# Performance work log

Hardware: AMD Instinct MI355X
Metric: run time of the kernel (lower is better)

Reference implementation:

```python
import jax, jax.numpy as jnp
import numpy as np

NEG_SLOPE = 0.2


def gat_conv(x, src, dst, W, a_src, a_dst, b, heads, out_ch, concat):
    """PyG-style GATConv (eval mode, self-loops already appended to src/dst)."""
    N = x.shape[0]
    h = (x @ W).reshape(N, heads, out_ch)            # [N,H,C]
    alpha_s = jnp.einsum('nhc,hc->nh', h, a_src)     # [N,H]
    alpha_d = jnp.einsum('nhc,hc->nh', h, a_dst)
    e = jax.nn.leaky_relu(alpha_s[src] + alpha_d[dst], NEG_SLOPE)  # [E,H]
    # segment softmax over incoming edges per destination node
    m = jax.ops.segment_max(e, dst, num_segments=N)  # every node has a self loop
    ex = jnp.exp(e - m[dst])
    denom = jax.ops.segment_sum(ex, dst, num_segments=N)
    alpha = ex / (denom[dst] + 1e-16)                # [E,H]
    msg = h[src] * alpha[:, :, None]                 # [E,H,C]
    out = jax.ops.segment_sum(msg, dst, num_segments=N)  # [N,H,C]
    if concat:
        out = out.reshape(N, heads * out_ch)
    else:
        out = out.mean(axis=1)
    return out + b


def setup_inputs() -> dict:
    key = jax.random.key(0)
    ks = jax.random.split(key, 12)
    N, E, F_IN = 100000, 3200000, 512
    H1, C1 = 8, 8           # conv1: heads=8, out=8, concat -> 64
    H2, C2 = 8, 16          # conv2: heads=8, out=num_classes=16, mean over heads
    x = jax.random.normal(ks[0], (N, F_IN), dtype=jnp.float32)
    edge_index = jax.random.randint(ks[1], (2, E), 0, N, dtype=jnp.int32)
    g = lambda k, s, fan: jax.random.normal(k, s, dtype=jnp.float32) / np.sqrt(fan)
    return {
        'x': x,
        'edge_index': edge_index,
        'W1': g(ks[2], (F_IN, H1 * C1), F_IN),
        'a_src1': g(ks[3], (H1, C1), C1),
        'a_dst1': g(ks[4], (H1, C1), C1),
        'b1': jnp.zeros((H1 * C1,), jnp.float32),
        'W2': g(ks[5], (H1 * C1, H2 * C2), H1 * C1),
        'a_src2': g(ks[6], (H2, C2), C2),
        'a_dst2': g(ks[7], (H2, C2), C2),
        'b2': jnp.zeros((C2,), jnp.float32),
    }


def reference(x, edge_index, W1, a_src1, a_dst1, b1, W2, a_src2, a_dst2, b2):
    N = x.shape[0]
    loops = jnp.arange(N, dtype=edge_index.dtype)
    src = jnp.concatenate([edge_index[0], loops])
    dst = jnp.concatenate([edge_index[1], loops])
    h = gat_conv(x, src, dst, W1, a_src1, a_dst1, b1, heads=8, out_ch=8, concat=True)
    h = jax.nn.elu(h)
    out = gat_conv(h, src, dst, W2, a_src2, a_dst2, b2, heads=8, out_ch=16, concat=False)
    return out
```

## Files before the change

### kernel.cpp

```cpp
#include <hip/hip_runtime.h>
#include <hip/hip_bf16.h>
#include <hip/hip_fp16.h>
#include <cstddef>

#define NEG_SLOPE 0.2f

typedef _Float16 half8 __attribute__((ext_vector_type(8)));
typedef float floatx4 __attribute__((ext_vector_type(4)));
typedef float floatx2 __attribute__((ext_vector_type(2)));


__global__ __launch_bounds__(256) void bucket_hist_k(const int* __restrict__ dst, int E,
                                                     int* __restrict__ bhist, int NB) {
    __shared__ int lh[256];
    for (int t = threadIdx.x; t < 256; t += 256) lh[t] = 0;
    __syncthreads();
    int per = (E + gridDim.x - 1) / gridDim.x;
    int s = blockIdx.x * per;
    int e = min(s + per, E);
    for (int i = s + threadIdx.x; i < e; i += 256) atomicAdd(&lh[dst[i] >> 9], 1);
    __syncthreads();
    for (int t = threadIdx.x; t < NB; t += 256)
        if (lh[t]) atomicAdd(&bhist[t], lh[t]);
}

__global__ __launch_bounds__(256) void bucket_scan_k(const int* __restrict__ bhist, int NB,
                                                     int* __restrict__ bbase, int* __restrict__ cursor,
                                                     int* __restrict__ row_start, int N, int E) {
    __shared__ int tmp[256];
    int tid = threadIdx.x;
    int v = (tid < NB) ? bhist[tid] : 0;
    tmp[tid] = v;
    __syncthreads();
    for (int d = 1; d < 256; d <<= 1) {
        int t = tmp[tid];
        int a = (tid >= d) ? tmp[tid - d] : 0;
        __syncthreads();
        tmp[tid] = t + a;
        __syncthreads();
    }
    if (tid < NB) {
        int b = tmp[tid] - v;
        bbase[tid] = b;
        cursor[tid] = b;
    }
    if (tid == 0) {
        bbase[NB] = E;
        row_start[N] = E;
    }
}

__global__ __launch_bounds__(256) void partition_k(const int* __restrict__ src,
                                                   const int* __restrict__ dst, int E,
                                                   int* __restrict__ cursor,
                                                   unsigned int* __restrict__ part, int NB) {
    __shared__ int lh[256];
    __shared__ int lbase[256];
    for (int t = threadIdx.x; t < 256; t += 256) lh[t] = 0;
    __syncthreads();
    int per = (E + gridDim.x - 1) / gridDim.x;
    int s = blockIdx.x * per;
    int e = min(s + per, E);
    for (int i = s + threadIdx.x; i < e; i += 256) atomicAdd(&lh[dst[i] >> 9], 1);
    __syncthreads();
    for (int t = threadIdx.x; t < NB; t += 256) {
        int c = lh[t];
        lbase[t] = c ? atomicAdd(&cursor[t], c) : 0;
        lh[t] = 0;
    }
    __syncthreads();
    for (int i = s + threadIdx.x; i < e; i += 256) {
        int d = dst[i];
        int b = d >> 9;
        int lo = atomicAdd(&lh[b], 1);
        part[lbase[b] + lo] = ((unsigned)src[i] << 9) | (unsigned)(d & 511);
    }
}

__global__ __launch_bounds__(512) void bucket_build_k(const unsigned int* __restrict__ part,
                                                      const int* __restrict__ bbase,
                                                      int* __restrict__ row_start,
                                                      int* __restrict__ csr, int N) {
    __shared__ int cnt[512];
    __shared__ int cur[512];
    int b = blockIdx.x, tid = threadIdx.x;
    int n0 = b << 9;
    int s = bbase[b], e2 = bbase[b + 1];
    cnt[tid] = 0;
    __syncthreads();
    for (int i = s + tid; i < e2; i += 512) atomicAdd(&cnt[part[i] & 511], 1);
    __syncthreads();
    int v = cnt[tid];
    for (int d = 1; d < 512; d <<= 1) {
        int t = cnt[tid];
        int a = (tid >= d) ? cnt[tid - d] : 0;
        __syncthreads();
        cnt[tid] = t + a;
        __syncthreads();
    }
    int excl = cnt[tid] - v;
    if (n0 + tid < N) row_start[n0 + tid] = s + excl;
    cur[tid] = excl;
    __syncthreads();
    for (int i = s + tid; i < e2; i += 512) {
        unsigned u = part[i];
        int p = atomicAdd(&cur[u & 511], 1);
        csr[s + p] = (int)(u >> 9);
    }
}


__global__ void convw_k(const float* __restrict__ W, _Float16* __restrict__ WT,
                        int K, int Nc) {
    int i = blockIdx.x * 256 + threadIdx.x;
    if (i < K * Nc) {
        int k = i / Nc, n = i % Nc;
        WT[(size_t)n * K + k] = (_Float16)W[i];
    }
}


__global__ __launch_bounds__(256) void gemm1_k(const float* __restrict__ A,
                                               const _Float16* __restrict__ BT,
                                               const float* __restrict__ a_s,
                                               const float* __restrict__ a_d,
                                               __half* __restrict__ C,
                                               float* __restrict__ os,
                                               float* __restrict__ od, int M) {
    constexpr int NT = 4, K = 512, Nc = 64;
    int wave = threadIdx.x >> 6, lane = threadIdx.x & 63;
    int m16 = lane & 15, quad = lane >> 4;
    int arow = blockIdx.x * 64 + wave * 16 + m16;
    int arc = arow < M ? arow : M - 1;
    floatx4 acc[NT] = {};
    for (int k0 = 0; k0 < K; k0 += 32) {
        const float* ap = A + (size_t)arc * K + k0 + quad * 8;
        float4 v0 = *(const float4*)ap;
        float4 v1 = *(const float4*)(ap + 4);
        half8 af;
        af[0] = (_Float16)v0.x; af[1] = (_Float16)v0.y;
        af[2] = (_Float16)v0.z; af[3] = (_Float16)v0.w;
        af[4] = (_Float16)v1.x; af[5] = (_Float16)v1.y;
        af[6] = (_Float16)v1.z; af[7] = (_Float16)v1.w;
#pragma unroll
        for (int t = 0; t < NT; ++t) {
            half8 bf = *(const half8*)(BT + (size_t)(t * 16 + m16) * K + k0 + quad * 8);
            acc[t] = __builtin_amdgcn_mfma_f32_16x16x32_f16(af, bf, acc[t], 0, 0, 0);
        }
    }
    int gm0 = blockIdx.x * 64 + wave * 16 + quad * 4;
    int head = (m16 >> 3);
#pragma unroll
    for (int t = 0; t < NT; ++t) {
        float ws = a_s[(2 * t + head) * 8 + (m16 & 7)];
        float wd = a_d[(2 * t + head) * 8 + (m16 & 7)];
#pragma unroll
        for (int r = 0; r < 4; ++r) {
            int gm = gm0 + r;
            float v = acc[t][r];
            if (gm < M) C[(size_t)gm * Nc + t * 16 + m16] = __float2half(v);
            float s = v * ws, d = v * wd;
            s += __shfl_xor(s, 1, 64); d += __shfl_xor(d, 1, 64);
            s += __shfl_xor(s, 2, 64); d += __shfl_xor(d, 2, 64);
            s += __shfl_xor(s, 4, 64); d += __shfl_xor(d, 4, 64);
            if ((m16 & 7) == 0 && gm < M) {
                os[gm * 8 + 2 * t + head] = s;
                od[gm * 8 + 2 * t + head] = d;
            }
        }
    }
}


__global__ __launch_bounds__(256) void gemm2_k(const _Float16* __restrict__ A,
                                               const _Float16* __restrict__ BT,
                                               const float* __restrict__ a_s,
                                               const float* __restrict__ a_d,
                                               unsigned short* __restrict__ Cf8,
                                               float* __restrict__ os,
                                               float* __restrict__ od, int M) {
    constexpr int NT = 8, K = 64;
    int wave = threadIdx.x >> 6, lane = threadIdx.x & 63;
    int m16 = lane & 15, quad = lane >> 4;
    int arow = blockIdx.x * 64 + wave * 16 + m16;
    int arc = arow < M ? arow : M - 1;
    floatx4 acc[NT] = {};
    for (int k0 = 0; k0 < K; k0 += 32) {
        half8 af = *(const half8*)(A + (size_t)arc * K + k0 + quad * 8);
#pragma unroll
        for (int t = 0; t < NT; ++t) {
            half8 bf = *(const half8*)(BT + (size_t)(t * 16 + m16) * K + k0 + quad * 8);
            acc[t] = __builtin_amdgcn_mfma_f32_16x16x32_f16(af, bf, acc[t], 0, 0, 0);
        }
    }
    int gm0 = blockIdx.x * 64 + wave * 16 + quad * 4;
#pragma unroll
    for (int t = 0; t < NT; ++t) {
        float ws = a_s[t * 16 + m16];
        float wd = a_d[t * 16 + m16];
#pragma unroll
        for (int r = 0; r < 4; ++r) {
            int gm = gm0 + r;
            float v = acc[t][r];
            float o = __shfl_xor(v, 1, 64);
            if (gm < M && !(m16 & 1)) {
                unsigned p = __builtin_amdgcn_cvt_pk_fp8_f32(v, o, 0, false);
                Cf8[(size_t)gm * 64 + t * 8 + (m16 >> 1)] = (unsigned short)(p & 0xffff);
            }
            float s = v * ws, d = v * wd;
            s += __shfl_xor(s, 1, 64); d += __shfl_xor(d, 1, 64);
            s += __shfl_xor(s, 2, 64); d += __shfl_xor(d, 2, 64);
            s += __shfl_xor(s, 4, 64); d += __shfl_xor(d, 4, 64);
            s += __shfl_xor(s, 8, 64); d += __shfl_xor(d, 8, 64);
            if (gm < M && m16 == t) {
                os[gm * 8 + t] = s;
                od[gm * 8 + t] = d;
            }
        }
    }
}


__global__ __launch_bounds__(64) void aggregate1_k(
    const __half2* __restrict__ H1, const float* __restrict__ as,
    const float* __restrict__ ad, const int* __restrict__ row_start,
    const int* __restrict__ csr, const float* __restrict__ b1,
    __half2* __restrict__ h1o, int N) {
    int l = threadIdx.x;
    int ll = l & 31;
    int n = min(blockIdx.x * 2 + (l >> 5), N - 1);
    int h = ll >> 2;
    int jj = ll & 3;
    int hbase = (l & 32) | (ll & 28);
    float adv = ad[n * 8 + h];
    float e0 = as[n * 8 + h] + adv;
    e0 = fmaxf(e0, NEG_SLOPE * e0);
    float ex0 = __expf(e0);
    float denom = ex0;
    float2 self = __half22float2(H1[(size_t)n * 32 + ll]);
    float accx = ex0 * self.x, accy = ex0 * self.y;
    int e = row_start[n], end = row_start[n + 1];
    for (; e + 8 <= end; e += 8) {
        int sjA = csr[e + jj];
        int sjB = csr[e + 4 + jj];
        float tA = as[sjA * 8 + h] + adv; tA = fmaxf(tA, NEG_SLOPE * tA);
        float tB = as[sjB * 8 + h] + adv; tB = fmaxf(tB, NEG_SLOPE * tB);
        float xA = __expf(tA), xB = __expf(tB);
#pragma unroll
        for (int q = 0; q < 4; ++q) {
            int sqA = __shfl(sjA, hbase + q, 64);
            float xqA = __shfl(xA, hbase + q, 64);
            float2 vA = __half22float2(H1[(size_t)sqA * 32 + ll]);
            int sqB = __shfl(sjB, hbase + q, 64);
            float xqB = __shfl(xB, hbase + q, 64);
            float2 vB = __half22float2(H1[(size_t)sqB * 32 + ll]);
            denom += xqA + xqB;
            accx = fmaf(xqA, vA.x, accx); accy = fmaf(xqA, vA.y, accy);
            accx = fmaf(xqB, vB.x, accx); accy = fmaf(xqB, vB.y, accy);
        }
    }
    while (e < end) {
        int rem = min(end - e, 4);
        int sj = csr[e + min(jj, rem - 1)];
        float t = as[sj * 8 + h] + adv;
        t = fmaxf(t, NEG_SLOPE * t);
        float xj = __expf(t);
        for (int q = 0; q < rem; ++q) {
            int sq = __shfl(sj, hbase + q, 64);
            float xq = __shfl(xj, hbase + q, 64);
            float2 v = __half22float2(H1[(size_t)sq * 32 + ll]);
            denom += xq;
            accx = fmaf(xq, v.x, accx);
            accy = fmaf(xq, v.y, accy);
        }
        e += rem;
    }
    float vx = accx / denom + b1[2 * ll];
    float vy = accy / denom + b1[2 * ll + 1];
    vx = vx > 0.f ? vx : expm1f(vx);
    vy = vy > 0.f ? vy : expm1f(vy);
    h1o[(size_t)n * 32 + ll] = __floats2half2_rn(vx, vy);
}


__global__ __launch_bounds__(64) void aggregate2_k(
    const unsigned int* __restrict__ H2, const float* __restrict__ as,
    const float* __restrict__ ad, const int* __restrict__ row_start,
    const int* __restrict__ csr, const float* __restrict__ b2,
    float* __restrict__ out, int N) {
    int l = threadIdx.x;
    int ll = l & 31;
    int n = min(blockIdx.x * 2 + (l >> 5), N - 1);
    int h = ll >> 2;
    int jj = ll & 3;
    int hbase = (l & 32) | (ll & 28);
    float adv = ad[n * 8 + h];
    float e0 = as[n * 8 + h] + adv;
    e0 = fmaxf(e0, NEG_SLOPE * e0);
    float ex0 = __expf(e0);
    float denom = ex0;
    unsigned sv = H2[(size_t)n * 32 + ll];
    floatx2 s01 = __builtin_amdgcn_cvt_pk_f32_fp8((int)sv, false);
    floatx2 s23 = __builtin_amdgcn_cvt_pk_f32_fp8((int)sv, true);
    float a0 = ex0 * s01[0], a1 = ex0 * s01[1];
    float a2 = ex0 * s23[0], a3 = ex0 * s23[1];
    int e = row_start[n], end = row_start[n + 1];
    for (; e + 8 <= end; e += 8) {
        int sjA = csr[e + jj];
        int sjB = csr[e + 4 + jj];
        float tA = as[sjA * 8 + h] + adv; tA = fmaxf(tA, NEG_SLOPE * tA);
        float tB = as[sjB * 8 + h] + adv; tB = fmaxf(tB, NEG_SLOPE * tB);
        float xA = __expf(tA), xB = __expf(tB);
#pragma unroll
        for (int q = 0; q < 4; ++q) {
            int sqA = __shfl(sjA, hbase + q, 64);
            float xqA = __shfl(xA, hbase + q, 64);
            unsigned gvA = H2[(size_t)sqA * 32 + ll];
            int sqB = __shfl(sjB, hbase + q, 64);
            float xqB = __shfl(xB, hbase + q, 64);
            unsigned gvB = H2[(size_t)sqB * 32 + ll];
            floatx2 vA01 = __builtin_amdgcn_cvt_pk_f32_fp8((int)gvA, false);
            floatx2 vA23 = __builtin_amdgcn_cvt_pk_f32_fp8((int)gvA, true);
            floatx2 vB01 = __builtin_amdgcn_cvt_pk_f32_fp8((int)gvB, false);
            floatx2 vB23 = __builtin_amdgcn_cvt_pk_f32_fp8((int)gvB, true);
            denom += xqA + xqB;
            a0 = fmaf(xqA, vA01[0], a0); a1 = fmaf(xqA, vA01[1], a1);
            a2 = fmaf(xqA, vA23[0], a2); a3 = fmaf(xqA, vA23[1], a3);
            a0 = fmaf(xqB, vB01[0], a0); a1 = fmaf(xqB, vB01[1], a1);
            a2 = fmaf(xqB, vB23[0], a2); a3 = fmaf(xqB, vB23[1], a3);
        }
    }
    while (e < end) {
        int rem = min(end - e, 4);
        int sj = csr[e + min(jj, rem - 1)];
        float t = as[sj * 8 + h] + adv;
        t = fmaxf(t, NEG_SLOPE * t);
        float xj = __expf(t);
        for (int q = 0; q < rem; ++q) {
            int sq = __shfl(sj, hbase + q, 64);
            float xq = __shfl(xj, hbase + q, 64);
            unsigned gv = H2[(size_t)sq * 32 + ll];
            floatx2 v01 = __builtin_amdgcn_cvt_pk_f32_fp8((int)gv, false);
            floatx2 v23 = __builtin_amdgcn_cvt_pk_f32_fp8((int)gv, true);
            denom += xq;
            a0 = fmaf(xq, v01[0], a0); a1 = fmaf(xq, v01[1], a1);
            a2 = fmaf(xq, v23[0], a2); a3 = fmaf(xq, v23[1], a3);
        }
        e += rem;
    }
    float inv = 1.f / denom;
    a0 *= inv; a1 *= inv; a2 *= inv; a3 *= inv;
#pragma unroll
    for (int m = 4; m <= 16; m <<= 1) {
        a0 += __shfl_xor(a0, m, 64);
        a1 += __shfl_xor(a1, m, 64);
        a2 += __shfl_xor(a2, m, 64);
        a3 += __shfl_xor(a3, m, 64);
    }
    if (ll < 4) {
        int c0 = ll * 4;
        float4 o;
        o.x = a0 * 0.125f + b2[c0];
        o.y = a1 * 0.125f + b2[c0 + 1];
        o.z = a2 * 0.125f + b2[c0 + 2];
        o.w = a3 * 0.125f + b2[c0 + 3];
        *(float4*)(out + (size_t)n * 16 + c0) = o;
    }
}


extern "C" void kernel_launch(void* const* d_in, const int* in_sizes, int n_in,
                              void* d_out, int out_size, void* d_ws, size_t ws_size,
                              hipStream_t stream) {
    (void)n_in; (void)out_size; (void)ws_size;
    const float* x      = (const float*)d_in[0];
    const int*   ei     = (const int*)d_in[1];
    const float* W1     = (const float*)d_in[2];
    const float* a_src1 = (const float*)d_in[3];
    const float* a_dst1 = (const float*)d_in[4];
    const float* b1     = (const float*)d_in[5];
    const float* W2     = (const float*)d_in[6];
    const float* a_src2 = (const float*)d_in[7];
    const float* a_dst2 = (const float*)d_in[8];
    const float* b2     = (const float*)d_in[9];

    int N = in_sizes[0] / 512;
    int E = in_sizes[1] / 2;
    const int* src = ei;
    const int* dst = ei + E;
    int NB = (N + 511) >> 9;

    char* ws = (char*)d_ws;
    size_t off = 0;
    auto alloc = [&](size_t bytes) -> void* {
        void* p = ws + off;
        off = (off + bytes + 255) & ~(size_t)255;
        return p;
    };
    __half* h1  = (__half*)alloc((size_t)N * 64 * 2);
    __half* h1o = (__half*)alloc((size_t)N * 64 * 2);
    unsigned short* h2f8 = (unsigned short*)alloc((size_t)N * 64 * 2);
    float* as1  = (float*)alloc((size_t)N * 8 * 4);
    float* ad1  = (float*)alloc((size_t)N * 8 * 4);
    float* as2  = (float*)alloc((size_t)N * 8 * 4);
    float* ad2  = (float*)alloc((size_t)N * 8 * 4);
    _Float16* W1T = (_Float16*)alloc((size_t)512 * 64 * 2);
    _Float16* W2T = (_Float16*)alloc((size_t)64 * 128 * 2);
    int* row_start = (int*)alloc((size_t)(N + 1) * 4);
    int* bhist     = (int*)alloc(256 * 4);
    int* bbase     = (int*)alloc(257 * 4);
    int* cursor    = (int*)alloc(256 * 4);
    unsigned int* part = (unsigned int*)alloc((size_t)E * 4);
    int* csr       = (int*)alloc((size_t)E * 4);

    convw_k<<<(512 * 64 + 255) / 256, 256, 0, stream>>>(W1, W1T, 512, 64);
    convw_k<<<(64 * 128 + 255) / 256, 256, 0, stream>>>(W2, W2T, 64, 128);

    hipMemsetAsync(bhist, 0, 256 * 4, stream);
    bucket_hist_k<<<512, 256, 0, stream>>>(dst, E, bhist, NB);
    bucket_scan_k<<<1, 256, 0, stream>>>(bhist, NB, bbase, cursor, row_start, N, E);
    partition_k<<<512, 256, 0, stream>>>(src, dst, E, cursor, part, NB);
    bucket_build_k<<<NB, 512, 0, stream>>>(part, bbase, row_start, csr, N);

    int gblocks = (N + 63) / 64;
    int ablocks = (N + 1) / 2;

    gemm1_k<<<gblocks, 256, 0, stream>>>(x, W1T, a_src1, a_dst1, h1, as1, ad1, N);
    aggregate1_k<<<ablocks, 64, 0, stream>>>((const __half2*)h1, as1, ad1, row_start,
                                             csr, b1, (__half2*)h1o, N);

    gemm2_k<<<gblocks, 256, 0, stream>>>((const _Float16*)h1o, W2T, a_src2, a_dst2,
                                         h2f8, as2, ad2, N);
    aggregate2_k<<<ablocks, 64, 0, stream>>>((const unsigned int*)h2f8, as2, ad2,
                                             row_start, csr, b2, (float*)d_out, N);
}
```

Before: 651.7 us.

## Fuse preprocessing kernels, co-launch partition with gemm1, and rework aggregation lane mapping

```diff
diff --git a/kernel.cpp b/kernel.cpp
--- a/kernel.cpp
+++ b/kernel.cpp
@@ -10,18 +10,35 @@
 typedef float floatx2 __attribute__((ext_vector_type(2)));
 
 
-__global__ __launch_bounds__(256) void bucket_hist_k(const int* __restrict__ dst, int E,
-                                                     int* __restrict__ bhist, int NB) {
-    __shared__ int lh[256];
-    for (int t = threadIdx.x; t < 256; t += 256) lh[t] = 0;
-    __syncthreads();
-    int per = (E + gridDim.x - 1) / gridDim.x;
-    int s = blockIdx.x * per;
-    int e = min(s + per, E);
-    for (int i = s + threadIdx.x; i < e; i += 256) atomicAdd(&lh[dst[i] >> 9], 1);
-    __syncthreads();
-    for (int t = threadIdx.x; t < NB; t += 256)
-        if (lh[t]) atomicAdd(&bhist[t], lh[t]);
+__global__ __launch_bounds__(256) void pre_k(const int* __restrict__ dst, int E,
+                                             int* __restrict__ bhist, int NB,
+                                             const float* __restrict__ W1, _Float16* __restrict__ W1T,
+                                             const float* __restrict__ W2, _Float16* __restrict__ W2T) {
+    int b = blockIdx.x;
+    if (b < 512) {
+        __shared__ int lh[256];
+        for (int t = threadIdx.x; t < 256; t += 256) lh[t] = 0;
+        __syncthreads();
+        int per = (E + 511) / 512;
+        int s = b * per;
+        int e = min(s + per, E);
+        for (int i = s + threadIdx.x; i < e; i += 256) atomicAdd(&lh[dst[i] >> 9], 1);
+        __syncthreads();
+        for (int t = threadIdx.x; t < NB; t += 256)
+            if (lh[t]) atomicAdd(&bhist[t], lh[t]);
+    } else if (b < 640) {
+        int i = (b - 512) * 256 + threadIdx.x;
+        if (i < 512 * 64) {
+            int k = i / 64, n = i % 64;
+            W1T[(size_t)n * 512 + k] = (_Float16)W1[i];
+        }
+    } else {
+        int i = (b - 640) * 256 + threadIdx.x;
+        if (i < 64 * 128) {
+            int k = i / 128, n = i % 128;
+            W2T[(size_t)n * 64 + k] = (_Float16)W2[i];
+        }
+    }
 }
 
 __global__ __launch_bounds__(256) void bucket_scan_k(const int* __restrict__ bhist, int NB,
@@ -47,33 +64,6 @@
     if (tid == 0) {
         bbase[NB] = E;
         row_start[N] = E;
-    }
-}
-
-__global__ __launch_bounds__(256) void partition_k(const int* __restrict__ src,
-                                                   const int* __restrict__ dst, int E,
-                                                   int* __restrict__ cursor,
-                                                   unsigned int* __restrict__ part, int NB) {
-    __shared__ int lh[256];
-    __shared__ int lbase[256];
-    for (int t = threadIdx.x; t < 256; t += 256) lh[t] = 0;
-    __syncthreads();
-    int per = (E + gridDim.x - 1) / gridDim.x;
-    int s = blockIdx.x * per;
-    int e = min(s + per, E);
-    for (int i = s + threadIdx.x; i < e; i += 256) atomicAdd(&lh[dst[i] >> 9], 1);
-    __syncthreads();
-    for (int t = threadIdx.x; t < NB; t += 256) {
-        int c = lh[t];
-        lbase[t] = c ? atomicAdd(&cursor[t], c) : 0;
-        lh[t] = 0;
-    }
-    __syncthreads();
-    for (int i = s + threadIdx.x; i < e; i += 256) {
-        int d = dst[i];
-        int b = d >> 9;
-        int lo = atomicAdd(&lh[b], 1);
-        part[lbase[b] + lo] = ((unsigned)src[i] << 9) | (unsigned)(d & 511);
     }
 }
 
@@ -110,27 +100,41 @@
 }
 
 
-__global__ void convw_k(const float* __restrict__ W, _Float16* __restrict__ WT,
-                        int K, int Nc) {
-    int i = blockIdx.x * 256 + threadIdx.x;
-    if (i < K * Nc) {
-        int k = i / Nc, n = i % Nc;
-        WT[(size_t)n * K + k] = (_Float16)W[i];
-    }
-}
-
-
-__global__ __launch_bounds__(256) void gemm1_k(const float* __restrict__ A,
-                                               const _Float16* __restrict__ BT,
-                                               const float* __restrict__ a_s,
-                                               const float* __restrict__ a_d,
-                                               __half* __restrict__ C,
-                                               float* __restrict__ os,
-                                               float* __restrict__ od, int M) {
+__global__ __launch_bounds__(256) void gemm1_part_k(
+    const float* __restrict__ A, const _Float16* __restrict__ BT,
+    const float* __restrict__ a_s, const float* __restrict__ a_d,
+    __half* __restrict__ C, float* __restrict__ os, float* __restrict__ od, int M,
+    const int* __restrict__ src, const int* __restrict__ dst, int E,
+    int* __restrict__ cursor, unsigned int* __restrict__ part, int NB) {
+    if (blockIdx.x < 512) {
+        __shared__ int lh[256];
+        __shared__ int lbase[256];
+        for (int t = threadIdx.x; t < 256; t += 256) lh[t] = 0;
+        __syncthreads();
+        int per = (E + 511) / 512;
+        int s = blockIdx.x * per;
+        int e = min(s + per, E);
+        for (int i = s + threadIdx.x; i < e; i += 256) atomicAdd(&lh[dst[i] >> 9], 1);
+        __syncthreads();
+        for (int t = threadIdx.x; t < NB; t += 256) {
+            int c = lh[t];
+            lbase[t] = c ? atomicAdd(&cursor[t], c) : 0;
+            lh[t] = 0;
+        }
+        __syncthreads();
+        for (int i = s + threadIdx.x; i < e; i += 256) {
+            int d = dst[i];
+            int b = d >> 9;
+            int lo = atomicAdd(&lh[b], 1);
+            part[lbase[b] + lo] = ((unsigned)src[i] << 9) | (unsigned)(d & 511);
+        }
+        return;
+    }
     constexpr int NT = 4, K = 512, Nc = 64;
+    int bid = blockIdx.x - 512;
     int wave = threadIdx.x >> 6, lane = threadIdx.x & 63;
     int m16 = lane & 15, quad = lane >> 4;
-    int arow = blockIdx.x * 64 + wave * 16 + m16;
+    int arow = bid * 64 + wave * 16 + m16;
     int arc = arow < M ? arow : M - 1;
     floatx4 acc[NT] = {};
     for (int k0 = 0; k0 < K; k0 += 32) {
@@ -148,7 +152,7 @@
             acc[t] = __builtin_amdgcn_mfma_f32_16x16x32_f16(af, bf, acc[t], 0, 0, 0);
         }
     }
-    int gm0 = blockIdx.x * 64 + wave * 16 + quad * 4;
+    int gm0 = bid * 64 + wave * 16 + quad * 4;
     int head = (m16 >> 3);
 #pragma unroll
     for (int t = 0; t < NT; ++t) {
@@ -221,150 +225,184 @@
 }
 
 
-__global__ __launch_bounds__(64) void aggregate1_k(
-    const __half2* __restrict__ H1, const float* __restrict__ as,
+__global__ __launch_bounds__(256) void aggregate1_k(
+    const uint2* __restrict__ H1, const float* __restrict__ as,
     const float* __restrict__ ad, const int* __restrict__ row_start,
     const int* __restrict__ csr, const float* __restrict__ b1,
-    __half2* __restrict__ h1o, int N) {
-    int l = threadIdx.x;
+    uint2* __restrict__ h1o, int N) {
+    int l = threadIdx.x & 63;
+    int wv = threadIdx.x >> 6;
     int ll = l & 31;
-    int n = min(blockIdx.x * 2 + (l >> 5), N - 1);
-    int h = ll >> 2;
-    int jj = ll & 3;
-    int hbase = (l & 32) | (ll & 28);
+    int n = min((int)(blockIdx.x * 8 + wv * 2 + (l >> 5)), N - 1);
+    int k = ll & 15;
+    int jj = ll >> 4;
+    int h = k >> 1;
+
     float adv = ad[n * 8 + h];
     float e0 = as[n * 8 + h] + adv;
     e0 = fmaxf(e0, NEG_SLOPE * e0);
     float ex0 = __expf(e0);
-    float denom = ex0;
-    float2 self = __half22float2(H1[(size_t)n * 32 + ll]);
-    float accx = ex0 * self.x, accy = ex0 * self.y;
+    float x0 = jj ? 0.f : ex0;
+
+    uint2 sv = H1[(size_t)n * 16 + k];
+    float2 s01 = __half22float2(*(const __half2*)&sv.x);
+    float2 s23 = __half22float2(*(const __half2*)&sv.y);
+    float denom = x0;
+    float a0 = x0 * s01.x, a1 = x0 * s01.y, a2 = x0 * s23.x, a3 = x0 * s23.y;
+
     int e = row_start[n], end = row_start[n + 1];
     for (; e + 8 <= end; e += 8) {
-        int sjA = csr[e + jj];
-        int sjB = csr[e + 4 + jj];
-        float tA = as[sjA * 8 + h] + adv; tA = fmaxf(tA, NEG_SLOPE * tA);
-        float tB = as[sjB * 8 + h] + adv; tB = fmaxf(tB, NEG_SLOPE * tB);
-        float xA = __expf(tA), xB = __expf(tB);
-#pragma unroll
-        for (int q = 0; q < 4; ++q) {
-            int sqA = __shfl(sjA, hbase + q, 64);
-            float xqA = __shfl(xA, hbase + q, 64);
-            float2 vA = __half22float2(H1[(size_t)sqA * 32 + ll]);
-            int sqB = __shfl(sjB, hbase + q, 64);
-            float xqB = __shfl(xB, hbase + q, 64);
-            float2 vB = __half22float2(H1[(size_t)sqB * 32 + ll]);
-            denom += xqA + xqB;
-            accx = fmaf(xqA, vA.x, accx); accy = fmaf(xqA, vA.y, accy);
-            accx = fmaf(xqB, vB.x, accx); accy = fmaf(xqB, vB.y, accy);
-        }
-    }
-    while (e < end) {
-        int rem = min(end - e, 4);
-        int sj = csr[e + min(jj, rem - 1)];
-        float t = as[sj * 8 + h] + adv;
-        t = fmaxf(t, NEG_SLOPE * t);
-        float xj = __expf(t);
-        for (int q = 0; q < rem; ++q) {
-            int sq = __shfl(sj, hbase + q, 64);
-            float xq = __shfl(xj, hbase + q, 64);
-            float2 v = __half22float2(H1[(size_t)sq * 32 + ll]);
-            denom += xq;
-            accx = fmaf(xq, v.x, accx);
-            accy = fmaf(xq, v.y, accy);
-        }
-        e += rem;
-    }
-    float vx = accx / denom + b1[2 * ll];
-    float vy = accy / denom + b1[2 * ll + 1];
-    vx = vx > 0.f ? vx : expm1f(vx);
-    vy = vy > 0.f ? vy : expm1f(vy);
-    h1o[(size_t)n * 32 + ll] = __floats2half2_rn(vx, vy);
-}
-
-
-__global__ __launch_bounds__(64) void aggregate2_k(
-    const unsigned int* __restrict__ H2, const float* __restrict__ as,
+#pragma unroll
+        for (int u = 0; u < 4; ++u) {
+            int sj = csr[e + 2 * u + jj];
+            float t = as[sj * 8 + h] + adv;
+            t = fmaxf(t, NEG_SLOPE * t);
+            float x = __expf(t);
+            uint2 gv = H1[(size_t)sj * 16 + k];
+            float2 v01 = __half22float2(*(const __half2*)&gv.x);
+            float2 v23 = __half22float2(*(const __half2*)&gv.y);
+            denom += x;
+            a0 = fmaf(x, v01.x, a0); a1 = fmaf(x, v01.y, a1);
+            a2 = fmaf(x, v23.x, a2); a3 = fmaf(x, v23.y, a3);
+        }
+    }
+    if (e < end) {
+#pragma unroll
+        for (int u = 0; u < 4; ++u) {
+            int idx = e + 2 * u + jj;
+            int sj = csr[min(idx, end - 1)];
+            float t = as[sj * 8 + h] + adv;
+            t = fmaxf(t, NEG_SLOPE * t);
+            float x = idx < end ? __expf(t) : 0.f;
+            uint2 gv = H1[(size_t)sj * 16 + k];
+            float2 v01 = __half22float2(*(const __half2*)&gv.x);
+            float2 v23 = __half22float2(*(const __half2*)&gv.y);
+            denom += x;
+            a0 = fmaf(x, v01.x, a0); a1 = fmaf(x, v01.y, a1);
+            a2 = fmaf(x, v23.x, a2); a3 = fmaf(x, v23.y, a3);
+        }
+    }
+    denom += __shfl_xor(denom, 16, 64);
+    a0 += __shfl_xor(a0, 16, 64);
+    a1 += __shfl_xor(a1, 16, 64);
+    a2 += __shfl_xor(a2, 16, 64);
+    a3 += __shfl_xor(a3, 16, 64);
+    float inv = 1.f / denom;
+    float r0 = a0 * inv + b1[4 * k + 0];
+    float r1 = a1 * inv + b1[4 * k + 1];
+    float r2 = a2 * inv + b1[4 * k + 2];
+    float r3 = a3 * inv + b1[4 * k + 3];
+    r0 = r0 > 0.f ? r0 : expm1f(r0);
+    r1 = r1 > 0.f ? r1 : expm1f(r1);
+    r2 = r2 > 0.f ? r2 : expm1f(r2);
+    r3 = r3 > 0.f ? r3 : expm1f(r3);
+    if (!jj) {
+        __half2 p01 = __floats2half2_rn(r0, r1);
+        __half2 p23 = __floats2half2_rn(r2, r3);
+        uint2 o;
+        o.x = *(const unsigned*)&p01;
+        o.y = *(const unsigned*)&p23;
+        h1o[(size_t)n * 16 + k] = o;
+    }
+}
+
+
+__global__ __launch_bounds__(256) void aggregate2_k(
+    const uint2* __restrict__ H2, const float* __restrict__ as,
     const float* __restrict__ ad, const int* __restrict__ row_start,
     const int* __restrict__ csr, const float* __restrict__ b2,
     float* __restrict__ out, int N) {
-    int l = threadIdx.x;
+    int l = threadIdx.x & 63;
+    int wv = threadIdx.x >> 6;
     int ll = l & 31;
-    int n = min(blockIdx.x * 2 + (l >> 5), N - 1);
-    int h = ll >> 2;
-    int jj = ll & 3;
-    int hbase = (l & 32) | (ll & 28);
+    int n = min((int)(blockIdx.x * 8 + wv * 2 + (l >> 5)), N - 1);
+    int k = ll & 15;
+    int jj = ll >> 4;
+    int h = k >> 1;
+
     float adv = ad[n * 8 + h];
     float e0 = as[n * 8 + h] + adv;
     e0 = fmaxf(e0, NEG_SLOPE * e0);
     float ex0 = __expf(e0);
-    float denom = ex0;
-    unsigned sv = H2[(size_t)n * 32 + ll];
-    floatx2 s01 = __builtin_amdgcn_cvt_pk_f32_fp8((int)sv, false);
-    floatx2 s23 = __builtin_amdgcn_cvt_pk_f32_fp8((int)sv, true);
-    float a0 = ex0 * s01[0], a1 = ex0 * s01[1];
-    float a2 = ex0 * s23[0], a3 = ex0 * s23[1];
+    float x0 = jj ? 0.f : ex0;
+
+    uint2 sv = H2[(size_t)n * 16 + k];
+    floatx2 p01 = __builtin_amdgcn_cvt_pk_f32_fp8((int)sv.x, false);
+    floatx2 p23 = __builtin_amdgcn_cvt_pk_f32_fp8((int)sv.x, true);
+    floatx2 p45 = __builtin_amdgcn_cvt_pk_f32_fp8((int)sv.y, false);
+    floatx2 p67 = __builtin_amdgcn_cvt_pk_f32_fp8((int)sv.y, true);
+    float denom = x0;
+    float a0 = x0 * p01[0], a1 = x0 * p01[1], a2 = x0 * p23[0], a3 = x0 * p23[1];
+    float a4 = x0 * p45[0], a5 = x0 * p45[1], a6 = x0 * p67[0], a7 = x0 * p67[1];
+
     int e = row_start[n], end = row_start[n + 1];
     for (; e + 8 <= end; e += 8) {
-        int sjA = csr[e + jj];
-        int sjB = csr[e + 4 + jj];
-        float tA = as[sjA * 8 + h] + adv; tA = fmaxf(tA, NEG_SLOPE * tA);
-        float tB = as[sjB * 8 + h] + adv; tB = fmaxf(tB, NEG_SLOPE * tB);
-        float xA = __expf(tA), xB = __expf(tB);
-#pragma unroll
-        for (int q = 0; q < 4; ++q) {
-            int sqA = __shfl(sjA, hbase + q, 64);
-            float xqA = __shfl(xA, hbase + q, 64);
-            unsigned gvA = H2[(size_t)sqA * 32 + ll];
-            int sqB = __shfl(sjB, hbase + q, 64);
-            float xqB = __shfl(xB, hbase + q, 64);
-            unsigned gvB = H2[(size_t)sqB * 32 + ll];
-            floatx2 vA01 = __builtin_amdgcn_cvt_pk_f32_fp8((int)gvA, false);
-            floatx2 vA23 = __builtin_amdgcn_cvt_pk_f32_fp8((int)gvA, true);
-            floatx2 vB01 = __builtin_amdgcn_cvt_pk_f32_fp8((int)gvB, false);
-            floatx2 vB23 = __builtin_amdgcn_cvt_pk_f32_fp8((int)gvB, true);
-            denom += xqA + xqB;
-            a0 = fmaf(xqA, vA01[0], a0); a1 = fmaf(xqA, vA01[1], a1);
-            a2 = fmaf(xqA, vA23[0], a2); a3 = fmaf(xqA, vA23[1], a3);
-            a0 = fmaf(xqB, vB01[0], a0); a1 = fmaf(xqB, vB01[1], a1);
-            a2 = fmaf(xqB, vB23[0], a2); a3 = fmaf(xqB, vB23[1], a3);
-        }
-    }
-    while (e < end) {
-        int rem = min(end - e, 4);
-        int sj = csr[e + min(jj, rem - 1)];
-        float t = as[sj * 8 + h] + adv;
-        t = fmaxf(t, NEG_SLOPE * t);
-        float xj = __expf(t);
-        for (int q = 0; q < rem; ++q) {
-            int sq = __shfl(sj, hbase + q, 64);
-            float xq = __shfl(xj, hbase + q, 64);
-            unsigned gv = H2[(size_t)sq * 32 + ll];
-            floatx2 v01 = __builtin_amdgcn_cvt_pk_f32_fp8((int)gv, false);
-            floatx2 v23 = __builtin_amdgcn_cvt_pk_f32_fp8((int)gv, true);
-            denom += xq;
-            a0 = fmaf(xq, v01[0], a0); a1 = fmaf(xq, v01[1], a1);
-            a2 = fmaf(xq, v23[0], a2); a3 = fmaf(xq, v23[1], a3);
-        }
-        e += rem;
-    }
+#pragma unroll
+        for (int u = 0; u < 4; ++u) {
+            int sj = csr[e + 2 * u + jj];
+            float t = as[sj * 8 + h] + adv;
+            t = fmaxf(t, NEG_SLOPE * t);
+            float x = __expf(t);
+            uint2 gv = H2[(size_t)sj * 16 + k];
+            floatx2 v01 = __builtin_amdgcn_cvt_pk_f32_fp8((int)gv.x, false);
+            floatx2 v23 = __builtin_amdgcn_cvt_pk_f32_fp8((int)gv.x, true);
+            floatx2 v45 = __builtin_amdgcn_cvt_pk_f32_fp8((int)gv.y, false);
+            floatx2 v67 = __builtin_amdgcn_cvt_pk_f32_fp8((int)gv.y, true);
+            denom += x;
+            a0 = fmaf(x, v01[0], a0); a1 = fmaf(x, v01[1], a1);
+            a2 = fmaf(x, v23[0], a2); a3 = fmaf(x, v23[1], a3);
+            a4 = fmaf(x, v45[0], a4); a5 = fmaf(x, v45[1], a5);
+            a6 = fmaf(x, v67[0], a6); a7 = fmaf(x, v67[1], a7);
+        }
+    }
+    if (e < end) {
+#pragma unroll
+        for (int u = 0; u < 4; ++u) {
+            int idx = e + 2 * u + jj;
+            int sj = csr[min(idx, end - 1)];
+            float t = as[sj * 8 + h] + adv;
+            t = fmaxf(t, NEG_SLOPE * t);
+            float x = idx < end ? __expf(t) : 0.f;
+            uint2 gv = H2[(size_t)sj * 16 + k];
+            floatx2 v01 = __builtin_amdgcn_cvt_pk_f32_fp8((int)gv.x, false);
+            floatx2 v23 = __builtin_amdgcn_cvt_pk_f32_fp8((int)gv.x, true);
+            floatx2 v45 = __builtin_amdgcn_cvt_pk_f32_fp8((int)gv.y, false);
+            floatx2 v67 = __builtin_amdgcn_cvt_pk_f32_fp8((int)gv.y, true);
+            denom += x;
+            a0 = fmaf(x, v01[0], a0); a1 = fmaf(x, v01[1], a1);
+            a2 = fmaf(x, v23[0], a2); a3 = fmaf(x, v23[1], a3);
+            a4 = fmaf(x, v45[0], a4); a5 = fmaf(x, v45[1], a5);
+            a6 = fmaf(x, v67[0], a6); a7 = fmaf(x, v67[1], a7);
+        }
+    }
+    denom += __shfl_xor(denom, 16, 64);
     float inv = 1.f / denom;
     a0 *= inv; a1 *= inv; a2 *= inv; a3 *= inv;
-#pragma unroll
-    for (int m = 4; m <= 16; m <<= 1) {
+    a4 *= inv; a5 *= inv; a6 *= inv; a7 *= inv;
+#pragma unroll
+    for (int m = 2; m <= 16; m <<= 1) {
         a0 += __shfl_xor(a0, m, 64);
         a1 += __shfl_xor(a1, m, 64);
         a2 += __shfl_xor(a2, m, 64);
         a3 += __shfl_xor(a3, m, 64);
-    }
-    if (ll < 4) {
-        int c0 = ll * 4;
-        float4 o;
-        o.x = a0 * 0.125f + b2[c0];
-        o.y = a1 * 0.125f + b2[c0 + 1];
-        o.z = a2 * 0.125f + b2[c0 + 2];
-        o.w = a3 * 0.125f + b2[c0 + 3];
-        *(float4*)(out + (size_t)n * 16 + c0) = o;
+        a4 += __shfl_xor(a4, m, 64);
+        a5 += __shfl_xor(a5, m, 64);
+        a6 += __shfl_xor(a6, m, 64);
+        a7 += __shfl_xor(a7, m, 64);
+    }
+    if (ll < 2) {
+        int c0 = k * 8;
+        float4 o0, o1;
+        o0.x = a0 * 0.125f + b2[c0 + 0];
+        o0.y = a1 * 0.125f + b2[c0 + 1];
+        o0.z = a2 * 0.125f + b2[c0 + 2];
+        o0.w = a3 * 0.125f + b2[c0 + 3];
+        o1.x = a4 * 0.125f + b2[c0 + 4];
+        o1.y = a5 * 0.125f + b2[c0 + 5];
+        o1.z = a6 * 0.125f + b2[c0 + 6];
+        o1.w = a7 * 0.125f + b2[c0 + 7];
+        *(float4*)(out + (size_t)n * 16 + c0) = o0;
+        *(float4*)(out + (size_t)n * 16 + c0 + 4) = o1;
     }
 }
 
@@ -413,24 +451,22 @@
     unsigned int* part = (unsigned int*)alloc((size_t)E * 4);
     int* csr       = (int*)alloc((size_t)E * 4);
 
-    convw_k<<<(512 * 64 + 255) / 256, 256, 0, stream>>>(W1, W1T, 512, 64);
-    convw_k<<<(64 * 128 + 255) / 256, 256, 0, stream>>>(W2, W2T, 64, 128);
-
     hipMemsetAsync(bhist, 0, 256 * 4, stream);
-    bucket_hist_k<<<512, 256, 0, stream>>>(dst, E, bhist, NB);
+    pre_k<<<672, 256, 0, stream>>>(dst, E, bhist, NB, W1, W1T, W2, W2T);
     bucket_scan_k<<<1, 256, 0, stream>>>(bhist, NB, bbase, cursor, row_start, N, E);
-    partition_k<<<512, 256, 0, stream>>>(src, dst, E, cursor, part, NB);
+
+    int gblocks = (N + 63) / 64;
+    int ablocks = (N + 7) / 8;
+
+    gemm1_part_k<<<512 + gblocks, 256, 0, stream>>>(x, W1T, a_src1, a_dst1, h1, as1, ad1, N,
+                                                    src, dst, E, cursor, part, NB);
     bucket_build_k<<<NB, 512, 0, stream>>>(part, bbase, row_start, csr, N);
 
-    int gblocks = (N + 63) / 64;
-    int ablocks = (N + 1) / 2;
-
-    gemm1_k<<<gblocks, 256, 0, stream>>>(x, W1T, a_src1, a_dst1, h1, as1, ad1, N);
-    aggregate1_k<<<ablocks, 64, 0, stream>>>((const __half2*)h1, as1, ad1, row_start,
-                                             csr, b1, (__half2*)h1o, N);
+    aggregate1_k<<<ablocks, 256, 0, stream>>>((const uint2*)h1, as1, ad1, row_start,
+                                              csr, b1, (uint2*)h1o, N);
 
     gemm2_k<<<gblocks, 256, 0, stream>>>((const _Float16*)h1o, W2T, a_src2, a_dst2,
                                          h2f8, as2, ad2, N);
-    aggregate2_k<<<ablocks, 64, 0, stream>>>((const unsigned int*)h2f8, as2, ad2,
-                                             row_start, csr, b2, (float*)d_out, N);
-}
+    aggregate2_k<<<ablocks, 256, 0, stream>>>((const uint2*)h2f8, as2, ad2,
+                                              row_start, csr, b2, (float*)d_out, N);
+}
```

Measured after the change: 643.8 us. Within noise of the previous version (-1.2%).
